# Optimization experiments

Hardware: AMD Instinct MI355X
Metric: run time of the kernel (lower is better)

The kernel has to match this reference:

```python
import jax, jax.numpy as jnp
import numpy as np

N = 100000       # nodes
E = 1600000      # edges
F_IN = 128       # num_features
DIM = 128        # hidden dim
L = 3            # num_gc_layers
G = 512          # num graphs
EPS = 1e-5       # BatchNorm eps


def setup_inputs() -> dict:
    key = jax.random.key(0)
    ks = jax.random.split(key, 3 + 4 * L)
    d = {
        "x": jax.random.normal(ks[0], (N, F_IN), jnp.float32),
        "edge_index": jax.random.randint(ks[1], (2, E), 0, N, dtype=jnp.int32).astype(jnp.int64),
        "batch": jnp.sort(jax.random.randint(ks[2], (N,), 0, G, dtype=jnp.int32)).astype(jnp.int64),
    }
    fin = F_IN
    for i in range(L):
        d[f"W{i}"] = jax.random.normal(ks[3 + 4 * i], (fin, DIM), jnp.float32) / np.float32(np.sqrt(fin))
        d[f"b{i}"] = jnp.zeros((DIM,), jnp.float32)
        d[f"g{i}"] = jnp.ones((DIM,), jnp.float32)   # BN gamma
        d[f"t{i}"] = jnp.zeros((DIM,), jnp.float32)  # BN beta
        fin = DIM
    return d


def _gcn_layer(h, src, dst, norm, W, b):
    # GCNConv: (xW) gathered at src, degree-normalized, scatter-added at dst, + bias
    h = h @ W                                    # [N, DIM] small GEMM
    msg = h[src] * norm[:, None]                 # [E+N, DIM] gather (memory-bound)
    out = jax.ops.segment_sum(msg, dst, num_segments=N)
    return out + b


def _forward(x, edge_index, batch, params):
    loops = jnp.arange(N, dtype=edge_index.dtype)
    src = jnp.concatenate([edge_index[0], loops])   # add self-loops (PyG default)
    dst = jnp.concatenate([edge_index[1], loops])
    deg = jax.ops.segment_sum(jnp.ones_like(src, jnp.float32), dst, num_segments=N)
    dinv = jax.lax.rsqrt(jnp.maximum(deg, 1.0))     # deg >= 1 due to self-loops
    norm = dinv[src] * dinv[dst]

    pools = []
    h = x
    for (W, b, g, t) in params:
        h = jax.nn.relu(_gcn_layer(h, src, dst, norm, W, b))
        # BatchNorm1d (training-mode batch stats, biased variance)
        mu = h.mean(axis=0)
        var = h.var(axis=0)
        h = (h - mu) * jax.lax.rsqrt(var + EPS) * g + t
        # global_add_pool per layer
        pools.append(jax.ops.segment_sum(h, batch, num_segments=G))
    return jnp.concatenate(pools, axis=1)  # [G, L*DIM]


def reference(x, edge_index, batch, W0, b0, g0, t0, W1, b1, g1, t1, W2, b2, g2, t2):
    params = [(W0, b0, g0, t0), (W1, b1, g1, t1), (W2, b2, g2, t2)]
    return _forward(x, edge_index, batch, params)
```

## Files before the change

kernel.cpp:

```cpp
#include <hip/hip_runtime.h>

#define NNODES 100000
#define NEDGES 1600000
#define NGRAPH 512
#define EPSBN 1e-5f
#define DEGCAP 64
#define NBUCK 512
#define BSH 8
#define BCAP 4864
#define P1_BLOCKS ((NEDGES + 4095)/4096)
#define GEMM_BLOCKS ((NNODES + 63)/64)

typedef unsigned short ushort_t;
typedef unsigned int uint_t;

typedef __attribute__((ext_vector_type(8))) __bf16 bf16x8;
typedef __attribute__((ext_vector_type(4))) float f32x4;
typedef __attribute__((ext_vector_type(2))) uint_t uintx2;

__device__ __forceinline__ float b2f(ushort_t u){ return __uint_as_float(((uint_t)u)<<16); }
__device__ __forceinline__ ushort_t f2b(float f){
  union { __bf16 h; ushort_t u; } c;
  c.h = (__bf16)f;
  return c.u;
}
__device__ __forceinline__ uint_t pkbf(float a, float b){
  union { __bf16 h[2]; uint_t u; } c;
  c.h[0] = (__bf16)a; c.h[1] = (__bf16)b;
  return c.u;
}
__device__ __forceinline__ float lo16(uint_t d){ return b2f((ushort_t)(d & 0xffffu)); }
__device__ __forceinline__ float hi16(uint_t d){ return b2f((ushort_t)(d >> 16)); }

__device__ __forceinline__ f32x4 mfma_bf16(bf16x8 a, bf16x8 b, f32x4 c){
  return __builtin_amdgcn_mfma_f32_16x16x32_bf16(a, b, c, 0, 0, 0);
}

union Frag8 { ushort_t u[8]; bf16x8 v; };

__device__ __forceinline__ bf16x8 cvt8_f32_bf16(const float* __restrict__ p){
  float4 v0 = *(const float4*)(const void*)p;
  float4 v1 = *(const float4*)(const void*)(p + 4);
  Frag8 f;
  f.u[0] = f2b(v0.x); f.u[1] = f2b(v0.y); f.u[2] = f2b(v0.z); f.u[3] = f2b(v0.w);
  f.u[4] = f2b(v1.x); f.u[5] = f2b(v1.y); f.u[6] = f2b(v1.z); f.u[7] = f2b(v1.w);
  return f.v;
}

__global__ __launch_bounds__(256) void k_p1(const int* __restrict__ src,
                                            const int* __restrict__ dst,
                                            int* __restrict__ gBucket,
                                            int2* __restrict__ ebuf,
                                            const int* __restrict__ batch,
                                            int* __restrict__ gstart){
  __shared__ int sMem[NBUCK*3];

  if (blockIdx.x < P1_BLOCKS){
    int* cntL  = sMem;
    int* baseL = cntL + NBUCK;
    int* ofsL  = baseL + NBUCK;
    int t = threadIdx.x;
    #pragma unroll
    for (int r = 0; r < 2; ++r){
      int i = t + r*256;
      cntL[i] = 0; ofsL[i] = 0;
    }
    __syncthreads();

    int base = blockIdx.x * 4096;
    int e0 = base + t*16;
    int s[16], d[16];
    int ne = 0;
    if (e0 + 16 <= NEDGES){
      #pragma unroll
      for (int q = 0; q < 4; ++q){
        int4 sv = *(const int4*)(src + e0 + q*4);
        int4 dv = *(const int4*)(dst + e0 + q*4);
        s[q*4+0]=sv.x; s[q*4+1]=sv.y; s[q*4+2]=sv.z; s[q*4+3]=sv.w;
        d[q*4+0]=dv.x; d[q*4+1]=dv.y; d[q*4+2]=dv.z; d[q*4+3]=dv.w;
      }
      ne = 16;
    } else {
      for (int e = e0; e < NEDGES && ne < 16; ++e, ++ne){
        s[ne] = src[e]; d[ne] = dst[e];
      }
    }
    for (int k = 0; k < ne; ++k) atomicAdd(&cntL[d[k] >> BSH], 1);
    __syncthreads();
    #pragma unroll
    for (int r = 0; r < 2; ++r){
      int i = t + r*256;
      int c = cntL[i];
      baseL[i] = c ? atomicAdd(&gBucket[i*16], c) : 0;
    }
    __syncthreads();
    for (int k = 0; k < ne; ++k){
      int b = d[k] >> BSH;
      int o = atomicAdd(&ofsL[b], 1);
      ebuf[(size_t)b*BCAP + baseL[b] + o] = make_int2(s[k], d[k]);
    }
    return;
  }
  #pragma unroll
  for (int r = 0; r < 2; ++r){
    int g = threadIdx.x + r*256;
    int lo = 0, hi = NNODES;
    while (lo < hi){
      int mid = (lo + hi) >> 1;
      if (batch[mid] < g) lo = mid + 1; else hi = mid;
    }
    gstart[g] = lo;
  }
  if (threadIdx.x == 0) gstart[NGRAPH] = NNODES;
}

__global__ __launch_bounds__(256) void k_p2(const int2* __restrict__ ebuf,
                                            const int* __restrict__ gBucket,
                                            int* __restrict__ colx,
                                            int* __restrict__ cnt){
  __shared__ int slotcnt[256];
  int t = threadIdx.x;
  int b = blockIdx.x;
  slotcnt[t] = 0;
  __syncthreads();

  int nb = gBucket[b*16];
  int vbase = b << BSH;

  for (int e = t; e < nb; e += 256){
    int2 p = ebuf[(size_t)b*BCAP + e];
    int slot = atomicAdd(&slotcnt[p.y - vbase], 1);
    colx[p.y*DEGCAP + slot] = p.x;
  }
  __syncthreads();

  int v = vbase + t;
  if (v < NNODES){
    int c = slotcnt[t];
    cnt[v] = c;
    int ce = (c <= 15) ? 15 : 31;
    for (int s = c; s < ce; ++s) colx[(size_t)v*DEGCAP + s] = NNODES;
  }
}

__global__ __launch_bounds__(256) void k_gemm0(const float* __restrict__ x,
                                               const float* __restrict__ W0,
                                               const int* __restrict__ cnt,
                                               ushort_t* __restrict__ hs){
  __shared__ __attribute__((aligned(16))) ushort_t sWT[128*136];
  for (int idx = threadIdx.x; idx < 128*128; idx += 256){
    int c = idx >> 7, jj = idx & 127;
    sWT[jj*136 + c] = f2b(W0[idx]);
  }
  __syncthreads();

  int wave = threadIdx.x >> 6;
  int lane = threadIdx.x & 63;
  int quad = lane >> 4;
  int l16  = lane & 15;
  int row0 = blockIdx.x*64 + wave*16;

  int m  = row0 + l16;
  int mc = (m < NNODES) ? m : (NNODES - 1);

  const float* ap = x + (size_t)mc*128 + quad*8;
  bf16x8 af0 = cvt8_f32_bf16(ap);
  bf16x8 af1 = cvt8_f32_bf16(ap + 32);
  bf16x8 af2 = cvt8_f32_bf16(ap + 64);
  bf16x8 af3 = cvt8_f32_bf16(ap + 96);

  f32x4 acc[8];
  #pragma unroll
  for (int ct = 0; ct < 8; ++ct){
    const ushort_t* bp = sWT + (ct*16 + l16)*136 + quad*8;
    bf16x8 b0 = *(const bf16x8*)(const void*)(bp);
    bf16x8 b1 = *(const bf16x8*)(const void*)(bp + 32);
    bf16x8 b2 = *(const bf16x8*)(const void*)(bp + 64);
    bf16x8 b3 = *(const bf16x8*)(const void*)(bp + 96);
    f32x4 a_ = {0.f, 0.f, 0.f, 0.f};
    a_ = mfma_bf16(af0, b0, a_);
    a_ = mfma_bf16(af1, b1, a_);
    a_ = mfma_bf16(af2, b2, a_);
    a_ = mfma_bf16(af3, b3, a_);
    acc[ct] = a_;
  }

  int rbase = row0 + quad*4;
  float dv[4];
  #pragma unroll
  for (int rg = 0; rg < 4; ++rg){
    int rr = rbase + rg;
    int cc = cnt[(rr < NNODES) ? rr : (NNODES - 1)];
    dv[rg] = rsqrtf((float)(cc + 1));
  }
  #pragma unroll
  for (int ct = 0; ct < 8; ++ct){
    int colc = ct*16 + l16;
    #pragma unroll
    for (int rg = 0; rg < 4; ++rg){
      int rr = rbase + rg;
      if (rr < NNODES) hs[(size_t)rr*128 + colc] = f2b(acc[ct][rg] * dv[rg]);
    }
  }
}

__global__ __launch_bounds__(256) void k_gemm(const ushort_t* __restrict__ A,
                                              const ushort_t* __restrict__ WT,
                                              const float* __restrict__ Kv,
                                              const int* __restrict__ cnt,
                                              ushort_t* __restrict__ hs){
  __shared__ __attribute__((aligned(16))) ushort_t sWT[128*136];
  {
    const uint4* sp = (const uint4*)WT;
    uint4* dp = (uint4*)sWT;
    for (int i = threadIdx.x; i < (128*136*2)/16; i += 256) dp[i] = sp[i];
  }
  __syncthreads();

  int wave = threadIdx.x >> 6;
  int lane = threadIdx.x & 63;
  int quad = lane >> 4;
  int l16  = lane & 15;
  int row0 = blockIdx.x*64 + wave*16;

  int m  = row0 + l16;
  int mc = (m < NNODES) ? m : (NNODES - 1);

  const ushort_t* ap = A + (size_t)mc*128 + quad*8;
  bf16x8 af0 = *(const bf16x8*)(const void*)(ap);
  bf16x8 af1 = *(const bf16x8*)(const void*)(ap + 32);
  bf16x8 af2 = *(const bf16x8*)(const void*)(ap + 64);
  bf16x8 af3 = *(const bf16x8*)(const void*)(ap + 96);

  f32x4 acc[8];
  #pragma unroll
  for (int ct = 0; ct < 8; ++ct){
    const ushort_t* bp = sWT + (ct*16 + l16)*136 + quad*8;
    bf16x8 b0 = *(const bf16x8*)(const void*)(bp);
    bf16x8 b1 = *(const bf16x8*)(const void*)(bp + 32);
    bf16x8 b2 = *(const bf16x8*)(const void*)(bp + 64);
    bf16x8 b3 = *(const bf16x8*)(const void*)(bp + 96);
    f32x4 a_ = {0.f, 0.f, 0.f, 0.f};
    a_ = mfma_bf16(af0, b0, a_);
    a_ = mfma_bf16(af1, b1, a_);
    a_ = mfma_bf16(af2, b2, a_);
    a_ = mfma_bf16(af3, b3, a_);
    acc[ct] = a_;
  }

  int rbase = row0 + quad*4;
  float dv[4];
  #pragma unroll
  for (int rg = 0; rg < 4; ++rg){
    int rr = rbase + rg;
    int cc = cnt[(rr < NNODES) ? rr : (NNODES - 1)];
    dv[rg] = rsqrtf((float)(cc + 1));
  }
  #pragma unroll
  for (int ct = 0; ct < 8; ++ct){
    int colc = ct*16 + l16;
    float kv = Kv[colc];
    #pragma unroll
    for (int rg = 0; rg < 4; ++rg){
      int rr = rbase + rg;
      if (rr < NNODES){
        float val = (acc[ct][rg] + kv) * dv[rg];
        hs[(size_t)rr*128 + colc] = f2b(val);
      }
    }
  }
}

#define AGG_BLOCKS 1024
#define AGG_WAVES (AGG_BLOCKS*4)
#define AGG_CHUNK ((NNODES + AGG_WAVES - 1) / AGG_WAVES)

#define FENCE8(A) asm volatile("" :: \
  "v"(A[0]),"v"(A[1]),"v"(A[2]),"v"(A[3]),"v"(A[4]),"v"(A[5]),"v"(A[6]),"v"(A[7]))

#define ISSUE_R0(dst, cr, vv) do { \
  _Pragma("unroll") \
  for (int k_ = 0; k_ < 8; ++k_){ \
    int uA_ = (k_ == 0) ? (vv) : __builtin_amdgcn_readlane((cr), 2*k_ - 1); \
    int uB_ = __builtin_amdgcn_readlane((cr), 2*k_); \
    int u_  = sel ? uB_ : uA_; \
    (dst)[k_] = H2[(uint_t)u_*32u + m]; \
  } \
} while(0)

#define ISSUE_R1(dst, cr) do { \
  _Pragma("unroll") \
  for (int k_ = 0; k_ < 8; ++k_){ \
    int uA_ = __builtin_amdgcn_readlane((cr), 15 + 2*k_); \
    int uB_ = __builtin_amdgcn_readlane((cr), 16 + 2*k_); \
    int u_  = sel ? uB_ : uA_; \
    (dst)[k_] = H2[(uint_t)u_*32u + m]; \
  } \
} while(0)

#define CONSUME8(A) do { \
  FENCE8(A); \
  _Pragma("unroll") \
  for (int k_ = 0; k_ < 8; ++k_){ \
    a0 += lo16((A)[k_].x); a1 += hi16((A)[k_].x); \
    a2 += lo16((A)[k_].y); a3 += hi16((A)[k_].y); \
  } \
} while(0)

template<bool WR>
__global__ __launch_bounds__(256, 4) void k_agg(const ushort_t* __restrict__ hs,
                                                const int* __restrict__ cnt,
                                                const int* __restrict__ colx,
                                                const float* __restrict__ bias,
                                                const int* __restrict__ batch,
                                                ushort_t* __restrict__ rout,
                                                float* __restrict__ poolS,
                                                float* __restrict__ chansum,
                                                float* __restrict__ chansumsq){
  __shared__ float bsum[128];
  __shared__ float bsq[128];
  if (threadIdx.x < 128){ bsum[threadIdx.x] = 0.f; bsq[threadIdx.x] = 0.f; }
  __syncthreads();

  int wave = __builtin_amdgcn_readfirstlane((blockIdx.x << 2) + (threadIdx.x >> 6));
  int lane = threadIdx.x & 63;
  int m    = lane & 31;
  int sel  = lane >> 5;
  int n0 = wave * AGG_CHUNK;
  int n1 = (n0 + AGG_CHUNK < NNODES) ? (n0 + AGG_CHUNK) : NNODES;

  const uintx2* H2 = (const uintx2*)hs;
  uintx2* R2 = (uintx2*)rout;

  float bbv[4];
  #pragma unroll
  for (int i = 0; i < 4; ++i) bbv[i] = bias[4*m + i];
  int chbase = 4*m + 2*sel;

  float ss0 = 0.f, ss1 = 0.f, sq0 = 0.f, sq1 = 0.f;
  float p0 = 0.f, p1 = 0.f;
  int curg = -1;

  if (n0 < n1){
    int cr0 = colx[(size_t)n0*DEGCAP + lane];
    int cv0 = cnt[n0];
    int cr1 = 0, cv1 = 0;
    if (n0 + 1 < n1){
      cr1 = colx[(size_t)(n0+1)*DEGCAP + lane];
      cv1 = cnt[n0+1];
    }
    uintx2 e0[8], e1[8];
    ISSUE_R0(e0, cr0, n0);
    if (cv0 > 15) ISSUE_R1(e1, cr0);
    else { _Pragma("unroll") for (int k_ = 0; k_ < 8; ++k_) e1[k_] = (uintx2){0u,0u}; }

    for (int v = n0; v < n1; ++v){
      int v2 = v + 2;
      int cr2 = 0, cv2 = 0;
      if (v2 < n1){
        cr2 = colx[(size_t)v2*DEGCAP + lane];
        cv2 = cnt[v2];
      }

      uintx2 f0[8], f1[8];
      bool hasn = (v + 1 < n1);
      if (hasn){
        ISSUE_R0(f0, cr1, v + 1);
        if (cv1 > 15) ISSUE_R1(f1, cr1);
        else { _Pragma("unroll") for (int k_ = 0; k_ < 8; ++k_) f1[k_] = (uintx2){0u,0u}; }
      } else {
        _Pragma("unroll") for (int k_ = 0; k_ < 8; ++k_){ f0[k_] = (uintx2){0u,0u}; f1[k_] = (uintx2){0u,0u}; }
      }

      int g = batch[v];
      if (g != curg){
        if (curg >= 0){
          atomicAdd(&poolS[curg*128 + chbase],     p0);
          atomicAdd(&poolS[curg*128 + chbase + 1], p1);
        }
        p0 = 0.f; p1 = 0.f; curg = g;
      }

      float a0 = 0.f, a1 = 0.f, a2 = 0.f, a3 = 0.f;

      CONSUME8(e0);
      if (cv0 > 15) CONSUME8(e1);
      if (cv0 > 31){
        for (int j = 31; j < cv0; j += 2){
          int uA = __builtin_amdgcn_readlane(cr0, j);
          int uB = (j + 1 < cv0) ? __builtin_amdgcn_readlane(cr0, j + 1) : NNODES;
          int u  = sel ? uB : uA;
          uintx2 dd = H2[(uint_t)u*32u + m];
          a0 += lo16(dd.x); a1 += hi16(dd.x);
          a2 += lo16(dd.y); a3 += hi16(dd.y);
        }
      }

      float s0 = a0 + __shfl_xor(a0, 32, 64);
      float s1 = a1 + __shfl_xor(a1, 32, 64);
      float s2 = a2 + __shfl_xor(a2, 32, 64);
      float s3 = a3 + __shfl_xor(a3, 32, 64);

      float dvv = rsqrtf((float)(cv0 + 1));
      float r0 = fmaxf(s0*dvv + bbv[0], 0.f);
      float r1 = fmaxf(s1*dvv + bbv[1], 0.f);
      float r2 = fmaxf(s2*dvv + bbv[2], 0.f);
      float r3 = fmaxf(s3*dvv + bbv[3], 0.f);
      if constexpr (WR){
        if (lane < 32){
          uintx2 wv;
          wv.x = pkbf(r0, r1);
          wv.y = pkbf(r2, r3);
          R2[(uint_t)v*32u + m] = wv;
        }
      }
      float cA = sel ? r2 : r0;
      float cB = sel ? r3 : r1;
      ss0 += cA; ss1 += cB;
      sq0 += cA*cA; sq1 += cB*cB;
      p0 += cA; p1 += cB;

      cr0 = cr1; cv0 = cv1;
      cr1 = cr2; cv1 = cv2;
      #pragma unroll
      for (int k_ = 0; k_ < 8; ++k_){ e0[k_] = f0[k_]; e1[k_] = f1[k_]; }
    }
  }

  if (curg >= 0){
    atomicAdd(&poolS[curg*128 + chbase],     p0);
    atomicAdd(&poolS[curg*128 + chbase + 1], p1);
  }
  atomicAdd(&bsum[chbase],     ss0);
  atomicAdd(&bsum[chbase + 1], ss1);
  atomicAdd(&bsq[chbase],      sq0);
  atomicAdd(&bsq[chbase + 1],  sq1);
  __syncthreads();
  if (threadIdx.x < 128){
    atomicAdd(&chansum[threadIdx.x],   bsum[threadIdx.x]);
    atomicAdd(&chansumsq[threadIdx.x], bsq[threadIdx.x]);
  }
}

__global__ void k_fold(const float* __restrict__ Wn,
                       const float* __restrict__ chansum, const float* __restrict__ chansumsq,
                       const float* __restrict__ gamma, const float* __restrict__ beta,
                       ushort_t* __restrict__ WT, float* __restrict__ Kv,
                       float* __restrict__ avec, float* __restrict__ cvec){
  __shared__ float red[128];
  int j = blockIdx.x, c = threadIdx.x;
  const float invN = 1.0f / (float)NNODES;
  float mu  = chansum[c] * invN;
  float var = chansumsq[c] * invN - mu*mu;
  float a = gamma[c] * rsqrtf(var + EPSBN);
  float cc = beta[c] - mu*a;
  if (j == 0){ avec[c] = a; cvec[c] = cc; }
  float wv = Wn[c*128 + j];
  WT[j*136 + c] = f2b(a * wv);
  red[c] = cc * wv;
  __syncthreads();
  for (int off = 64; off > 0; off >>= 1){
    if (c < off) red[c] += red[c + off];
    __syncthreads();
  }
  if (c == 0) Kv[j] = red[0];
}

__global__ void k_final(const float* __restrict__ poolS, const int* __restrict__ gstart,
                        const float* __restrict__ avec, const float* __restrict__ cvec,
                        const float* __restrict__ chansum2, const float* __restrict__ chansumsq2,
                        const float* __restrict__ gamma2, const float* __restrict__ beta2,
                        float* __restrict__ out){
  int g = blockIdx.x, c = threadIdx.x;
  float n = (float)(gstart[g + 1] - gstart[g]);
  #pragma unroll
  for (int i = 0; i < 2; ++i){
    float v = avec[i*128 + c] * poolS[((size_t)i*NGRAPH + g)*128 + c] + n * cvec[i*128 + c];
    out[(size_t)g*384 + i*128 + c] = v;
  }
  const float invN = 1.0f / (float)NNODES;
  float mu  = chansum2[c] * invN;
  float var = chansumsq2[c] * invN - mu*mu;
  float a2 = gamma2[c] * rsqrtf(var + EPSBN);
  float c2 = beta2[c] - mu*a2;
  float v2 = a2 * poolS[((size_t)2*NGRAPH + g)*128 + c] + n * c2;
  out[(size_t)g*384 + 2*128 + c] = v2;
}

extern "C" void kernel_launch(void* const* d_in, const int* in_sizes, int n_in,
                              void* d_out, int out_size, void* d_ws, size_t ws_size,
                              hipStream_t stream){
  (void)in_sizes; (void)n_in; (void)out_size; (void)ws_size;

  const float* x     = (const float*)d_in[0];
  const int*   ei    = (const int*)d_in[1];
  const int*   batch = (const int*)d_in[2];
  const float* Wp[3] = {(const float*)d_in[3], (const float*)d_in[7],  (const float*)d_in[11]};
  const float* bp[3] = {(const float*)d_in[4], (const float*)d_in[8],  (const float*)d_in[12]};
  const float* gp[3] = {(const float*)d_in[5], (const float*)d_in[9],  (const float*)d_in[13]};
  const float* tp[3] = {(const float*)d_in[6], (const float*)d_in[10], (const float*)d_in[14]};
  const int* srcp = ei;
  const int* dstp = ei + NEDGES;

  char* w = (char*)d_ws;
  size_t off = 0;
  auto take = [&](size_t bytes) -> char* {
    char* p = w + off;
    off += (bytes + 511) & ~(size_t)511;
    return p;
  };
  int*      cnt       = (int*)take((size_t)NNODES*4);
  int*      colx      = (int*)take((size_t)NNODES*DEGCAP*4);
  int*      gstart    = (int*)take((NGRAPH+1)*4);
  ushort_t* hs        = (ushort_t*)take((size_t)(NNODES+1)*128*2);
  ushort_t* rbuf      = (ushort_t*)take((size_t)NNODES*128*2);
  ushort_t* WT        = (ushort_t*)take(128*136*2);
  float*    Kv        = (float*)take(128*4);
  float*    chanstats = (float*)take(3*256*4);
  float*    poolS     = (float*)take((size_t)3*NGRAPH*128*4);
  float*    avec      = (float*)take(2*128*4);
  float*    cvec      = (float*)take(2*128*4);
  int*      gBucket   = (int*)take(NBUCK*16*4);

  int2* ebuf = (int2*)rbuf;

  hipMemsetAsync(gBucket,   0, NBUCK*16*4,             stream);
  hipMemsetAsync(poolS,     0, (size_t)3*NGRAPH*128*4, stream);
  hipMemsetAsync(chanstats, 0, 3*256*4,                stream);
  hipMemsetAsync(hs + (size_t)NNODES*128, 0, 128*2,    stream);

  k_p1<<<P1_BLOCKS + 1, 256, 0, stream>>>(srcp, dstp, gBucket, ebuf, batch, gstart);
  k_p2<<<NBUCK, 256, 0, stream>>>(ebuf, gBucket, colx, cnt);
  k_gemm0<<<GEMM_BLOCKS, 256, 0, stream>>>(x, Wp[0], cnt, hs);

  k_agg<true><<<AGG_BLOCKS, 256, 0, stream>>>(hs, cnt, colx, bp[0], batch, rbuf,
                                              poolS, chanstats, chanstats + 128);
  k_fold<<<128, 128, 0, stream>>>(Wp[1], chanstats, chanstats + 128,
                                  gp[0], tp[0], WT, Kv, avec, cvec);
  k_gemm<<<GEMM_BLOCKS, 256, 0, stream>>>(rbuf, WT, Kv, cnt, hs);
  k_agg<true><<<AGG_BLOCKS, 256, 0, stream>>>(hs, cnt, colx, bp[1], batch, rbuf,
                                              poolS + (size_t)NGRAPH*128,
                                              chanstats + 256, chanstats + 256 + 128);
  k_fold<<<128, 128, 0, stream>>>(Wp[2], chanstats + 256, chanstats + 256 + 128,
                                  gp[1], tp[1], WT, Kv, avec + 128, cvec + 128);
  k_gemm<<<GEMM_BLOCKS, 256, 0, stream>>>(rbuf, WT, Kv, cnt, hs);
  k_agg<false><<<AGG_BLOCKS, 256, 0, stream>>>(hs, cnt, colx, bp[2], batch, rbuf,
                                               poolS + (size_t)2*NGRAPH*128,
                                               chanstats + 512, chanstats + 512 + 128);

  k_final<<<NGRAPH, 128, 0, stream>>>(poolS, gstart, avec, cvec,
                                      chanstats + 512, chanstats + 512 + 128,
                                      gp[2], tp[2], (float*)d_out);
}
```

Baseline: 441.9 us.

## Fuse BN-fold into GEMM, merge memsets, move graph-start search into final

Removes the separate k_fold launches by having each GEMM block recompute the BatchNorm scale/shift and fold them into the bf16 weight tile in shared memory, with Kv accumulated through shared atomics. Merges the four memsets into one contiguous memset plus an in-kernel zeroing of the padding row. Moves the per-graph binary search from k_p1 into k_final. The intent is fewer launches and less serialization; the cost is that every GEMM block now converts fp32 weights and does 16K shared atomics.

```diff
diff --git a/kernel.cpp b/kernel.cpp
--- a/kernel.cpp
+++ b/kernel.cpp
@@ -50,68 +50,51 @@
 __global__ __launch_bounds__(256) void k_p1(const int* __restrict__ src,
                                             const int* __restrict__ dst,
                                             int* __restrict__ gBucket,
-                                            int2* __restrict__ ebuf,
-                                            const int* __restrict__ batch,
-                                            int* __restrict__ gstart){
+                                            int2* __restrict__ ebuf){
   __shared__ int sMem[NBUCK*3];
-
-  if (blockIdx.x < P1_BLOCKS){
-    int* cntL  = sMem;
-    int* baseL = cntL + NBUCK;
-    int* ofsL  = baseL + NBUCK;
-    int t = threadIdx.x;
+  int* cntL  = sMem;
+  int* baseL = cntL + NBUCK;
+  int* ofsL  = baseL + NBUCK;
+  int t = threadIdx.x;
+  #pragma unroll
+  for (int r = 0; r < 2; ++r){
+    int i = t + r*256;
+    cntL[i] = 0; ofsL[i] = 0;
+  }
+  __syncthreads();
+
+  int base = blockIdx.x * 4096;
+  int e0 = base + t*16;
+  int s[16], d[16];
+  int ne = 0;
+  if (e0 + 16 <= NEDGES){
     #pragma unroll
-    for (int r = 0; r < 2; ++r){
-      int i = t + r*256;
-      cntL[i] = 0; ofsL[i] = 0;
-    }
-    __syncthreads();
-
-    int base = blockIdx.x * 4096;
-    int e0 = base + t*16;
-    int s[16], d[16];
-    int ne = 0;
-    if (e0 + 16 <= NEDGES){
-      #pragma unroll
-      for (int q = 0; q < 4; ++q){
-        int4 sv = *(const int4*)(src + e0 + q*4);
-        int4 dv = *(const int4*)(dst + e0 + q*4);
-        s[q*4+0]=sv.x; s[q*4+1]=sv.y; s[q*4+2]=sv.z; s[q*4+3]=sv.w;
-        d[q*4+0]=dv.x; d[q*4+1]=dv.y; d[q*4+2]=dv.z; d[q*4+3]=dv.w;
-      }
-      ne = 16;
-    } else {
-      for (int e = e0; e < NEDGES && ne < 16; ++e, ++ne){
-        s[ne] = src[e]; d[ne] = dst[e];
-      }
-    }
-    for (int k = 0; k < ne; ++k) atomicAdd(&cntL[d[k] >> BSH], 1);
-    __syncthreads();
-    #pragma unroll
-    for (int r = 0; r < 2; ++r){
-      int i = t + r*256;
-      int c = cntL[i];
-      baseL[i] = c ? atomicAdd(&gBucket[i*16], c) : 0;
-    }
-    __syncthreads();
-    for (int k = 0; k < ne; ++k){
-      int b = d[k] >> BSH;
-      int o = atomicAdd(&ofsL[b], 1);
-      ebuf[(size_t)b*BCAP + baseL[b] + o] = make_int2(s[k], d[k]);
-    }
-    return;
-  }
+    for (int q = 0; q < 4; ++q){
+      int4 sv = *(const int4*)(src + e0 + q*4);
+      int4 dv = *(const int4*)(dst + e0 + q*4);
+      s[q*4+0]=sv.x; s[q*4+1]=sv.y; s[q*4+2]=sv.z; s[q*4+3]=sv.w;
+      d[q*4+0]=dv.x; d[q*4+1]=dv.y; d[q*4+2]=dv.z; d[q*4+3]=dv.w;
+    }
+    ne = 16;
+  } else {
+    for (int e = e0; e < NEDGES && ne < 16; ++e, ++ne){
+      s[ne] = src[e]; d[ne] = dst[e];
+    }
+  }
+  for (int k = 0; k < ne; ++k) atomicAdd(&cntL[d[k] >> BSH], 1);
+  __syncthreads();
   #pragma unroll
   for (int r = 0; r < 2; ++r){
-    int g = threadIdx.x + r*256;
-    int lo = 0, hi = NNODES;
-    while (lo < hi){
-      int mid = (lo + hi) >> 1;
-      if (batch[mid] < g) lo = mid + 1; else hi = mid;
-    }
-    gstart[g] = lo;
-  }
-  if (threadIdx.x == 0) gstart[NGRAPH] = NNODES;
+    int i = t + r*256;
+    int c = cntL[i];
+    baseL[i] = c ? atomicAdd(&gBucket[i*16], c) : 0;
+  }
+  __syncthreads();
+  for (int k = 0; k < ne; ++k){
+    int b = d[k] >> BSH;
+    int o = atomicAdd(&ofsL[b], 1);
+    ebuf[(size_t)b*BCAP + baseL[b] + o] = make_int2(s[k], d[k]);
+  }
 }
 
 __global__ __launch_bounds__(256) void k_p2(const int2* __restrict__ ebuf,
@@ -148,6 +131,8 @@
                                                const int* __restrict__ cnt,
                                                ushort_t* __restrict__ hs){
   __shared__ __attribute__((aligned(16))) ushort_t sWT[128*136];
+  if (blockIdx.x == 0 && threadIdx.x < 64)
+    ((uint_t*)hs)[(size_t)NNODES*64 + threadIdx.x] = 0u;
   for (int idx = threadIdx.x; idx < 128*128; idx += 256){
     int c = idx >> 7, jj = idx & 127;
     sWT[jj*136 + c] = f2b(W0[idx]);
@@ -204,21 +189,40 @@
   }
 }
 
-__global__ __launch_bounds__(256) void k_gemm(const ushort_t* __restrict__ A,
-                                              const ushort_t* __restrict__ WT,
-                                              const float* __restrict__ Kv,
-                                              const int* __restrict__ cnt,
-                                              ushort_t* __restrict__ hs){
+__global__ __launch_bounds__(256) void k_gemmf(const ushort_t* __restrict__ A,
+                                               const float* __restrict__ Wn,
+                                               const float* __restrict__ chansum,
+                                               const float* __restrict__ chansumsq,
+                                               const float* __restrict__ gamma,
+                                               const float* __restrict__ beta,
+                                               const int* __restrict__ cnt,
+                                               ushort_t* __restrict__ hs){
   __shared__ __attribute__((aligned(16))) ushort_t sWT[128*136];
-  {
-    const uint4* sp = (const uint4*)WT;
-    uint4* dp = (uint4*)sWT;
-    for (int i = threadIdx.x; i < (128*136*2)/16; i += 256) dp[i] = sp[i];
-  }
-  __syncthreads();
-
-  int wave = threadIdx.x >> 6;
-  int lane = threadIdx.x & 63;
+  __shared__ float aL[128];
+  __shared__ float cL[128];
+  __shared__ float KvL[128];
+
+  int t = threadIdx.x;
+  if (t < 128){
+    const float invN = 1.0f / (float)NNODES;
+    float mu  = chansum[t] * invN;
+    float var = chansumsq[t] * invN - mu*mu;
+    float a = gamma[t] * rsqrtf(var + EPSBN);
+    aL[t] = a;
+    cL[t] = beta[t] - mu*a;
+    KvL[t] = 0.f;
+  }
+  __syncthreads();
+  for (int idx = t; idx < 128*128; idx += 256){
+    int c = idx >> 7, jj = idx & 127;
+    float wv = Wn[idx];
+    sWT[jj*136 + c] = f2b(aL[c] * wv);
+    atomicAdd(&KvL[jj], cL[c] * wv);
+  }
+  __syncthreads();
+
+  int wave = t >> 6;
+  int lane = t & 63;
   int quad = lane >> 4;
   int l16  = lane & 15;
   int row0 = blockIdx.x*64 + wave*16;
@@ -259,7 +263,7 @@
   #pragma unroll
   for (int ct = 0; ct < 8; ++ct){
     int colc = ct*16 + l16;
-    float kv = Kv[colc];
+    float kv = KvL[colc];
     #pragma unroll
     for (int rg = 0; rg < 4; ++rg){
       int rr = rbase + rg;
@@ -442,49 +446,39 @@
   }
 }
 
-__global__ void k_fold(const float* __restrict__ Wn,
-                       const float* __restrict__ chansum, const float* __restrict__ chansumsq,
-                       const float* __restrict__ gamma, const float* __restrict__ beta,
-                       ushort_t* __restrict__ WT, float* __restrict__ Kv,
-                       float* __restrict__ avec, float* __restrict__ cvec){
-  __shared__ float red[128];
-  int j = blockIdx.x, c = threadIdx.x;
+__global__ void k_final(const float* __restrict__ poolS,
+                        const int* __restrict__ batch,
+                        const float* __restrict__ chanstats,
+                        const float* __restrict__ g0, const float* __restrict__ t0,
+                        const float* __restrict__ g1, const float* __restrict__ t1,
+                        const float* __restrict__ g2, const float* __restrict__ t2,
+                        float* __restrict__ out){
+  __shared__ int s_n[2];
+  int g = blockIdx.x, c = threadIdx.x;
+  if (c < 2){
+    int target = g + c;
+    int lo = 0, hi = NNODES;
+    while (lo < hi){
+      int mid = (lo + hi) >> 1;
+      if (batch[mid] < target) lo = mid + 1; else hi = mid;
+    }
+    s_n[c] = lo;
+  }
+  __syncthreads();
+  float n = (float)(s_n[1] - s_n[0]);
+
+  const float* gam[3] = {g0, g1, g2};
+  const float* bet[3] = {t0, t1, t2};
   const float invN = 1.0f / (float)NNODES;
-  float mu  = chansum[c] * invN;
-  float var = chansumsq[c] * invN - mu*mu;
-  float a = gamma[c] * rsqrtf(var + EPSBN);
-  float cc = beta[c] - mu*a;
-  if (j == 0){ avec[c] = a; cvec[c] = cc; }
-  float wv = Wn[c*128 + j];
-  WT[j*136 + c] = f2b(a * wv);
-  red[c] = cc * wv;
-  __syncthreads();
-  for (int off = 64; off > 0; off >>= 1){
-    if (c < off) red[c] += red[c + off];
-    __syncthreads();
-  }
-  if (c == 0) Kv[j] = red[0];
-}
-
-__global__ void k_final(const float* __restrict__ poolS, const int* __restrict__ gstart,
-                        const float* __restrict__ avec, const float* __restrict__ cvec,
-                        const float* __restrict__ chansum2, const float* __restrict__ chansumsq2,
-                        const float* __restrict__ gamma2, const float* __restrict__ beta2,
-                        float* __restrict__ out){
-  int g = blockIdx.x, c = threadIdx.x;
-  float n = (float)(gstart[g + 1] - gstart[g]);
-  #pragma unroll
-  for (int i = 0; i < 2; ++i){
-    float v = avec[i*128 + c] * poolS[((size_t)i*NGRAPH + g)*128 + c] + n * cvec[i*128 + c];
+  #pragma unroll
+  for (int i = 0; i < 3; ++i){
+    float mu  = chanstats[i*256 + c] * invN;
+    float var = chanstats[i*256 + 128 + c] * invN - mu*mu;
+    float a = gam[i][c] * rsqrtf(var + EPSBN);
+    float cc = bet[i][c] - mu*a;
+    float v = a * poolS[((size_t)i*NGRAPH + g)*128 + c] + n * cc;
     out[(size_t)g*384 + i*128 + c] = v;
   }
-  const float invN = 1.0f / (float)NNODES;
-  float mu  = chansum2[c] * invN;
-  float var = chansumsq2[c] * invN - mu*mu;
-  float a2 = gamma2[c] * rsqrtf(var + EPSBN);
-  float c2 = beta2[c] - mu*a2;
-  float v2 = a2 * poolS[((size_t)2*NGRAPH + g)*128 + c] + n * c2;
-  out[(size_t)g*384 + 2*128 + c] = v2;
 }
 
 extern "C" void kernel_launch(void* const* d_in, const int* in_sizes, int n_in,
@@ -511,44 +505,38 @@
   };
   int*      cnt       = (int*)take((size_t)NNODES*4);
   int*      colx      = (int*)take((size_t)NNODES*DEGCAP*4);
-  int*      gstart    = (int*)take((NGRAPH+1)*4);
   ushort_t* hs        = (ushort_t*)take((size_t)(NNODES+1)*128*2);
   ushort_t* rbuf      = (ushort_t*)take((size_t)NNODES*128*2);
-  ushort_t* WT        = (ushort_t*)take(128*136*2);
-  float*    Kv        = (float*)take(128*4);
-  float*    chanstats = (float*)take(3*256*4);
-  float*    poolS     = (float*)take((size_t)3*NGRAPH*128*4);
-  float*    avec      = (float*)take(2*128*4);
-  float*    cvec      = (float*)take(2*128*4);
-  int*      gBucket   = (int*)take(NBUCK*16*4);
+  const size_t ZB_GB = (size_t)NBUCK*16*4;
+  const size_t ZB_CS = 3*256*4;
+  const size_t ZB_PS = (size_t)3*NGRAPH*128*4;
+  char* zbase = take(ZB_GB + ZB_CS + ZB_PS);
+  int*   gBucket   = (int*)zbase;
+  float* chanstats = (float*)(zbase + ZB_GB);
+  float* poolS     = (float*)(zbase + ZB_GB + ZB_CS);
 
   int2* ebuf = (int2*)rbuf;
 
-  hipMemsetAsync(gBucket,   0, NBUCK*16*4,             stream);
-  hipMemsetAsync(poolS,     0, (size_t)3*NGRAPH*128*4, stream);
-  hipMemsetAsync(chanstats, 0, 3*256*4,                stream);
-  hipMemsetAsync(hs + (size_t)NNODES*128, 0, 128*2,    stream);
-
-  k_p1<<<P1_BLOCKS + 1, 256, 0, stream>>>(srcp, dstp, gBucket, ebuf, batch, gstart);
+  hipMemsetAsync(zbase, 0, ZB_GB + ZB_CS + ZB_PS, stream);
+
+  k_p1<<<P1_BLOCKS, 256, 0, stream>>>(srcp, dstp, gBucket, ebuf);
   k_p2<<<NBUCK, 256, 0, stream>>>(ebuf, gBucket, colx, cnt);
   k_gemm0<<<GEMM_BLOCKS, 256, 0, stream>>>(x, Wp[0], cnt, hs);
 
   k_agg<true><<<AGG_BLOCKS, 256, 0, stream>>>(hs, cnt, colx, bp[0], batch, rbuf,
                                               poolS, chanstats, chanstats + 128);
-  k_fold<<<128, 128, 0, stream>>>(Wp[1], chanstats, chanstats + 128,
-                                  gp[0], tp[0], WT, Kv, avec, cvec);
-  k_gemm<<<GEMM_BLOCKS, 256, 0, stream>>>(rbuf, WT, Kv, cnt, hs);
+  k_gemmf<<<GEMM_BLOCKS, 256, 0, stream>>>(rbuf, Wp[1], chanstats, chanstats + 128,
+                                           gp[0], tp[0], cnt, hs);
   k_agg<true><<<AGG_BLOCKS, 256, 0, stream>>>(hs, cnt, colx, bp[1], batch, rbuf,
                                               poolS + (size_t)NGRAPH*128,
                                               chanstats + 256, chanstats + 256 + 128);
-  k_fold<<<128, 128, 0, stream>>>(Wp[2], chanstats + 256, chanstats + 256 + 128,
-                                  gp[1], tp[1], WT, Kv, avec + 128, cvec + 128);
-  k_gemm<<<GEMM_BLOCKS, 256, 0, stream>>>(rbuf, WT, Kv, cnt, hs);
+  k_gemmf<<<GEMM_BLOCKS, 256, 0, stream>>>(rbuf, Wp[2], chanstats + 256, chanstats + 256 + 128,
+                                           gp[1], tp[1], cnt, hs);
   k_agg<false><<<AGG_BLOCKS, 256, 0, stream>>>(hs, cnt, colx, bp[2], batch, rbuf,
                                                poolS + (size_t)2*NGRAPH*128,
                                                chanstats + 512, chanstats + 512 + 128);
 
-  k_final<<<NGRAPH, 128, 0, stream>>>(poolS, gstart, avec, cvec,
-                                      chanstats + 512, chanstats + 512 + 128,
-                                      gp[2], tp[2], (float*)d_out);
-}
+  k_final<<<NGRAPH, 128, 0, stream>>>(poolS, batch, chanstats,
+                                      gp[0], tp[0], gp[1], tp[1], gp[2], tp[2],
+                                      (float*)d_out);
+}
```

New measurement: 711.2 us. 60.9% more time.
